# Kernel tuning notes

Hardware: AMD Instinct MI355X
Metric: run time of the kernel (lower is better)

Reference implementation:

```python
import jax, jax.numpy as jnp
import numpy as np

N_HEAD = 16
EPS = 1e-6

def hypersphere_norm(x, g):
    # unit-normalize on hidden dim, rescale to sqrt(d), learnable gain
    d = x.shape[-1]
    n = jnp.linalg.norm(x, axis=-1, keepdims=True)
    return (x / (n + EPS)) * jnp.sqrt(jnp.asarray(d, x.dtype)) * g


def setup_inputs() -> dict:
    key = jax.random.key(0)
    ks = jax.random.split(key, 8)
    B, S, D, F = 2, 2048, 2048, 8192
    s = lambda fan: 1.0 / np.sqrt(fan)
    return {
        "hidden_states": jax.random.normal(ks[0], (B, S, D), jnp.float32),
        "Wq": jax.random.normal(ks[1], (D, D), jnp.float32) * s(D),
        "Wk": jax.random.normal(ks[2], (D, D), jnp.float32) * s(D),
        "Wv": jax.random.normal(ks[3], (D, D), jnp.float32) * s(D),
        "Wo": jax.random.normal(ks[4], (D, D), jnp.float32) * s(D),
        "W_in": jax.random.normal(ks[5], (F, D), jnp.float32) * s(D),
        "W_out": jax.random.normal(ks[6], (D, F), jnp.float32) * s(F),
        "qk_norm_factor": jnp.asarray(1.0 / np.sqrt(D // N_HEAD), jnp.float32),
        "g_attn": jnp.ones((D,), jnp.float32),
        "g_mlp": jnp.ones((D,), jnp.float32),
    }


def reference(hidden_states, Wq, Wk, Wv, Wo, W_in, W_out, qk_norm_factor, g_attn, g_mlp):
    B, S, D = hidden_states.shape
    H = N_HEAD
    hd = D // H

    # ---- pre-attn hypersphere norm ----
    residual = hidden_states
    x = hypersphere_norm(hidden_states, g_attn)

    def shape_heads(t):  # [B,S,D] -> [B,H,S,hd]
        return t.reshape(B, S, H, hd).transpose(0, 2, 1, 3)

    q = shape_heads(x @ Wq.T)
    k = shape_heads(x @ Wk.T)
    v = shape_heads(x @ Wv.T)

    # QK-norm: unit-normalize per head vector
    q = q / (jnp.linalg.norm(q, axis=-1, keepdims=True) + EPS)
    k = k / (jnp.linalg.norm(k, axis=-1, keepdims=True) + EPS)

    scores = jnp.einsum("bhqd,bhkd->bhqk", q, k) * qk_norm_factor
    causal = jnp.tril(jnp.ones((S, S), bool))
    scores = jnp.where(causal[None, None], scores, jnp.asarray(-jnp.inf, scores.dtype))
    probs = jax.nn.softmax(scores, axis=-1)
    attn = jnp.einsum("bhqk,bhkd->bhqd", probs, v)  # [B,H,S,hd]
    attn = attn.transpose(0, 2, 1, 3).reshape(B, S, D)
    attn = attn @ Wo.T  # dropout=0

    h = residual + attn

    # ---- MLP branch ----
    residual = h
    y = hypersphere_norm(h, g_mlp)
    y = jax.nn.gelu(y @ W_in.T, approximate=False)
    y = y @ W_out.T
    return residual + y
```

## Files before the change

### kernel.cpp

```cpp
#include <hip/hip_runtime.h>
#include <math.h>


typedef unsigned short ushort_t;
typedef __attribute__((ext_vector_type(8))) short short8;
typedef __attribute__((ext_vector_type(4))) short short4v;
typedef __attribute__((ext_vector_type(4))) float f32x4;

#define S_LEN 2048
#define D_DIM 2048
#define F_DIM 8192
#define NHEAD 16
#define HDIM 128
#define BATCH 2
#define MROWS (BATCH * S_LEN)

__device__ __forceinline__ float bf2f(ushort_t u) {
  union { unsigned int i; float f; } c; c.i = ((unsigned int)u) << 16; return c.f;
}
__device__ __forceinline__ ushort_t f2bf(float f) {
  union { unsigned int i; float f; } c; c.f = f;
  unsigned int u = c.i;
  unsigned int r = (u + 0x7FFFu + ((u >> 16) & 1u)) >> 16;
  return (ushort_t)r;
}
__device__ __forceinline__ void load_lds16(const ushort_t* g, ushort_t* l) {
  __builtin_amdgcn_global_load_lds((const __attribute__((address_space(1))) void*)g,
                                   (__attribute__((address_space(3))) void*)l,
                                   16, 0, 0);
}
__device__ __forceinline__ f32x4 mf(short8 a, short8 b, f32x4 c) {
  return __builtin_amdgcn_mfma_f32_16x16x32_bf16(a, b, c, 0, 0, 0);
}

__global__ __launch_bounds__(256) void f2b_all_kernel(const float* __restrict__ wq,
                                                      const float* __restrict__ wk,
                                                      const float* __restrict__ wv,
                                                      const float* __restrict__ wo,
                                                      const float* __restrict__ wi,
                                                      const float* __restrict__ wu,
                                                      ushort_t* __restrict__ out) {
  const size_t DD = (size_t)D_DIM * D_DIM;
  const size_t FD = (size_t)F_DIM * D_DIM;
  const size_t e = ((size_t)blockIdx.x * 256 + threadIdx.x) * 4;
  const float* src;
  size_t off;
  if (e < 4 * DD) {
    const int wsel = (int)(e >> 22);
    src = (wsel == 0) ? wq : (wsel == 1) ? wk : (wsel == 2) ? wv : wo;
    off = e & (DD - 1);
  } else if (e < 4 * DD + FD) {
    src = wi; off = e - 4 * DD;
  } else {
    src = wu; off = e - 4 * DD - FD;
  }
  float4 v = *(const float4*)(src + off);
  short4v o;
  o[0] = (short)f2bf(v.x); o[1] = (short)f2bf(v.y);
  o[2] = (short)f2bf(v.z); o[3] = (short)f2bf(v.w);
  *(short4v*)(out + e) = o;
}

__global__ __launch_bounds__(256) void hsnorm_kernel(const float* __restrict__ x,
                                                     const float* __restrict__ g,
                                                     ushort_t* __restrict__ out) {
  const int row = blockIdx.x;
  const int t = threadIdx.x;
  const size_t base = (size_t)row * D_DIM + t * 8;
  float4 x0 = *(const float4*)(x + base);
  float4 x1 = *(const float4*)(x + base + 4);
  float f[8] = {x0.x, x0.y, x0.z, x0.w, x1.x, x1.y, x1.z, x1.w};
  float ss = 0.f;
#pragma unroll
  for (int j = 0; j < 8; ++j) ss += f[j] * f[j];
#pragma unroll
  for (int o = 32; o >= 1; o >>= 1) ss += __shfl_xor(ss, o);
  __shared__ float red[4];
  if ((t & 63) == 0) red[t >> 6] = ss;
  __syncthreads();
  const float tot = red[0] + red[1] + red[2] + red[3];
  const float factor = 45.254833995939045f / (sqrtf(tot) + 1e-6f);
  float4 g0 = *(const float4*)(g + t * 8);
  float4 g1 = *(const float4*)(g + t * 8 + 4);
  float gg[8] = {g0.x, g0.y, g0.z, g0.w, g1.x, g1.y, g1.z, g1.w};
  short8 ov;
#pragma unroll
  for (int j = 0; j < 8; ++j) ov[j] = (short)f2bf(f[j] * factor * gg[j]);
  *(short8*)(out + base) = ov;
}

__global__ __launch_bounds__(256) void qknorm_kernel(ushort_t* __restrict__ buf, float scale) {
  const int wv = threadIdx.x >> 6;
  const int lane = threadIdx.x & 63;
  const size_t vi = (size_t)blockIdx.x * 4 + wv;
  ushort_t* p = buf + vi * 128 + lane * 2;
  const float a = bf2f(p[0]), b = bf2f(p[1]);
  float ss = a * a + b * b;
#pragma unroll
  for (int o = 32; o >= 1; o >>= 1) ss += __shfl_xor(ss, o);
  const float f = scale / (sqrtf(ss) + 1e-6f);
  p[0] = f2bf(a * f);
  p[1] = f2bf(b * f);
}

template <int EPI>
__global__ __launch_bounds__(512, 2) void gemm256(const ushort_t* __restrict__ A,
                                                  const ushort_t* __restrict__ W,
                                                  const float* __restrict__ RES,
                                                  void* __restrict__ Cv,
                                                  int M, int N, int K) {
  extern __shared__ char smem[];
  const int tid = threadIdx.x;
  const int w = tid >> 6;
  const int lane = tid & 63;
  const int quad = lane >> 4;
  const int l15 = lane & 15;
  const int wr = w >> 2, wc = w & 3;

  const int bid = blockIdx.x;
  const int cpx = gridDim.x >> 3;
  const int wg = (bid & 7) * cpx + (bid >> 3);
  const long bm = (long)(wg & 15) * 256;
  const long bn = (long)(wg >> 4) * 256;

  const int rx = (l15 >> 1) & 3;
  const int a_base = ((wr * 128 + l15) << 6) + ((quad ^ rx) << 4);
  const int b_base = ((wc * 64 + l15) << 6) + ((quad ^ rx) << 4);

  const int sp = (((tid & 3) ^ ((tid >> 3) & 3)) << 3);
  const int srow = tid >> 2;
  const ushort_t* gA = A + (size_t)(bm + srow) * K + sp;
  const ushort_t* gB = W + (size_t)(bn + srow) * K + sp;
  const size_t rstep = (size_t)128 * K;
  const int sdst = w * 1024;

#define STAGE(BI, STEP)                                                     \
  {                                                                         \
    char* ab = smem + (BI)*16384;                                           \
    char* bb = smem + 65536 + (BI)*16384;                                   \
    const ushort_t* ga = gA + (size_t)(STEP) * 32;                          \
    const ushort_t* gb = gB + (size_t)(STEP) * 32;                          \
    load_lds16(ga, (ushort_t*)(ab + sdst));                                 \
    load_lds16(ga + rstep, (ushort_t*)(ab + 8192 + sdst));                  \
    load_lds16(gb, (ushort_t*)(bb + sdst));                                 \
    load_lds16(gb + rstep, (ushort_t*)(bb + 8192 + sdst));                  \
  }

  f32x4 acc[8][4] = {};
  short8 af[4], bf[4];
  const int NT = K >> 5;

  STAGE(0, 0);
  STAGE(1, 1);
  STAGE(2, 2);
  asm volatile("s_waitcnt vmcnt(8)" ::: "memory");
  __builtin_amdgcn_s_barrier();

  for (int s = 0; s < NT; ++s) {
    const char* sa = smem + (s & 3) * 16384;
    const char* sb = smem + 65536 + (s & 3) * 16384;
#pragma unroll
    for (int j = 0; j < 4; ++j) bf[j] = *(const short8*)(sb + b_base + j * 1024);
#pragma unroll
    for (int i = 0; i < 4; ++i) af[i] = *(const short8*)(sa + a_base + i * 1024);
    if (s + 3 < NT) STAGE((s + 3) & 3, s + 3);
    __builtin_amdgcn_s_setprio(1);
#pragma unroll
    for (int i = 0; i < 4; ++i)
#pragma unroll
      for (int j = 0; j < 4; ++j) acc[i][j] = mf(af[i], bf[j], acc[i][j]);
    __builtin_amdgcn_s_setprio(0);
#pragma unroll
    for (int i = 0; i < 4; ++i) af[i] = *(const short8*)(sa + a_base + (4 + i) * 1024);
    __builtin_amdgcn_s_setprio(1);
#pragma unroll
    for (int i = 0; i < 4; ++i)
#pragma unroll
      for (int j = 0; j < 4; ++j) acc[4 + i][j] = mf(af[i], bf[j], acc[4 + i][j]);
    __builtin_amdgcn_s_setprio(0);
    if (s < NT - 3) {
      asm volatile("s_waitcnt vmcnt(8)" ::: "memory");
    } else if (s == NT - 3) {
      asm volatile("s_waitcnt vmcnt(4)" ::: "memory");
    } else {
      asm volatile("s_waitcnt vmcnt(0)" ::: "memory");
    }
    __builtin_amdgcn_s_barrier();
  }
#undef STAGE

  const size_t SZq = (size_t)MROWS * D_DIM;
#pragma unroll
  for (int i = 0; i < 8; ++i) {
    const long row0 = bm + wr * 128 + i * 16 + quad * 4;
#pragma unroll
    for (int j = 0; j < 4; ++j) {
      const long col = bn + wc * 64 + j * 16 + l15;
      if (EPI == 4) {
        if (col < 4096) {
          ushort_t* dst = (ushort_t*)Cv + (col < 2048 ? 0 : SZq);
          const long c = col & (D_DIM - 1);
#pragma unroll
          for (int r = 0; r < 4; ++r)
            dst[(size_t)(row0 + r) * D_DIM + c] = f2bf(acc[i][j][r]);
        } else {
          const long b = row0 >> 11;
          const long s0 = row0 & (S_LEN - 1);
          const long h = (col >> 7) & 15;
          const long d = col & (HDIM - 1);
          short4v ov;
#pragma unroll
          for (int r = 0; r < 4; ++r) ov[r] = (short)f2bf(acc[i][j][r]);
          *(short4v*)((ushort_t*)Cv + 2 * SZq + ((b * NHEAD + h) * HDIM + d) * S_LEN + s0) = ov;
        }
      } else {
#pragma unroll
        for (int r = 0; r < 4; ++r) {
          float v = acc[i][j][r];
          const size_t idx = (size_t)(row0 + r) * N + col;
          if (EPI == 1) {
            ((float*)Cv)[idx] = v + RES[idx];
          } else if (EPI == 2) {
            v = 0.5f * v * (1.0f + erff(v * 0.70710678118654752f));
            ((ushort_t*)Cv)[idx] = f2bf(v);
          }
        }
      }
    }
  }
}

__global__ __launch_bounds__(256) void attn_kernel(const ushort_t* __restrict__ q,
                                                   const ushort_t* __restrict__ k,
                                                   const ushort_t* __restrict__ vt,
                                                   ushort_t* __restrict__ out) {
  __shared__ __align__(16) ushort_t K_lds[64 * 128];
  __shared__ __align__(16) ushort_t Vt_lds[128 * 64];
  __shared__ __align__(16) ushort_t P_lds[4 * 16 * 64];
  const int tid = threadIdx.x;
  const int w = tid >> 6;
  const int lane = tid & 63;
  const int quad = lane >> 4;
  const int l15 = lane & 15;

  const int qt = (S_LEN / 64 - 1) - (blockIdx.x & (S_LEN / 64 - 1));
  const int bh = blockIdx.x >> 5;
  const int b = bh >> 4;
  const int h = bh & 15;
  const int q0 = qt * 64;
  const int wrow0 = q0 + w * 16;
  const size_t base = ((size_t)b * S_LEN) * D_DIM + h * HDIM;
  const size_t vtbase = ((size_t)(b * NHEAD + h)) * HDIM * S_LEN;

  short8 qa[4];
#pragma unroll
  for (int st = 0; st < 4; ++st)
    qa[st] = *(const short8*)(q + base + (size_t)(wrow0 + l15) * D_DIM + st * 32 + quad * 8);

  const int kc0 = w * 64 + lane;
  ushort_t* Pw = P_lds + w * 1024;

  f32x4 o[8] = {};
  float m[4], l[4];
#pragma unroll
  for (int r = 0; r < 4; ++r) { m[r] = -__builtin_inff(); l[r] = 0.f; }

  const int ktmax = (q0 + 63) >> 6;
  for (int kt = 0; kt <= ktmax; ++kt) {
#pragma unroll
    for (int r2 = 0; r2 < 4; ++r2) {
      const int c = r2 * 256 + kc0;
      {
        const int db = c >> 8, key = (c >> 2) & 63, dl = (c & 3) * 8;
        load_lds16(k + base + (size_t)(kt * 64 + key) * D_DIM + db * 32 + dl,
                   K_lds + (size_t)(r2 * 4 + w) * 512);
      }
      {
        const int kc = c >> 9, d = (c >> 2) & 127, kl = (c & 3) * 8;
        load_lds16(vt + vtbase + (size_t)d * S_LEN + kt * 64 + kc * 32 + kl,
                   Vt_lds + (size_t)(r2 * 4 + w) * 512);
      }
    }
    __syncthreads();

    if (kt * 64 <= wrow0 + 15) {
      f32x4 s[4];
#pragma unroll
      for (int h2 = 0; h2 < 4; ++h2) {
        f32x4 sa = {};
#pragma unroll
        for (int st = 0; st < 4; ++st) {
          short8 kb = *(const short8*)&K_lds[st * 2048 + (h2 * 16 + l15) * 32 + quad * 8];
          sa = __builtin_amdgcn_mfma_f32_16x16x32_bf16(qa[st], kb, sa, 0, 0, 0);
        }
        s[h2] = sa;
      }

      const int kbase = kt * 64 + l15;
      float alpha[4];
#pragma unroll
      for (int r = 0; r < 4; ++r) {
        const int qrow = wrow0 + quad * 4 + r;
        float sv[4];
#pragma unroll
        for (int h2 = 0; h2 < 4; ++h2)
          sv[h2] = (kbase + h2 * 16 <= qrow) ? s[h2][r] : -__builtin_inff();
        float tmax = fmaxf(fmaxf(sv[0], sv[1]), fmaxf(sv[2], sv[3]));
#pragma unroll
        for (int off = 8; off >= 1; off >>= 1) tmax = fmaxf(tmax, __shfl_xor(tmax, off));
        const float mn = fmaxf(m[r], tmax);
        const float al = __expf(m[r] - mn);
        float p[4], ps = 0.f;
#pragma unroll
        for (int h2 = 0; h2 < 4; ++h2) { p[h2] = __expf(sv[h2] - mn); ps += p[h2]; }
#pragma unroll
        for (int off = 8; off >= 1; off >>= 1) ps += __shfl_xor(ps, off);
        l[r] = l[r] * al + ps;
        m[r] = mn;
        alpha[r] = al;
#pragma unroll
        for (int h2 = 0; h2 < 4; ++h2)
          Pw[(h2 >> 1) * 512 + (quad * 4 + r) * 32 + (h2 & 1) * 16 + l15] = f2bf(p[h2]);
      }

#pragma unroll
      for (int c = 0; c < 8; ++c)
#pragma unroll
        for (int r = 0; r < 4; ++r) o[c][r] *= alpha[r];

      short8 af0 = *(const short8*)&Pw[l15 * 32 + quad * 8];
      short8 af1 = *(const short8*)&Pw[512 + l15 * 32 + quad * 8];
#pragma unroll
      for (int c = 0; c < 8; ++c) {
        short8 vb0 = *(const short8*)&Vt_lds[(c * 16 + l15) * 32 + quad * 8];
        o[c] = __builtin_amdgcn_mfma_f32_16x16x32_bf16(af0, vb0, o[c], 0, 0, 0);
        short8 vb1 = *(const short8*)&Vt_lds[4096 + (c * 16 + l15) * 32 + quad * 8];
        o[c] = __builtin_amdgcn_mfma_f32_16x16x32_bf16(af1, vb1, o[c], 0, 0, 0);
      }
    }
    __syncthreads();
  }

#pragma unroll
  for (int c = 0; c < 8; ++c)
#pragma unroll
    for (int r = 0; r < 4; ++r) {
      const float val = o[c][r] / l[r];
      out[base + (size_t)(wrow0 + quad * 4 + r) * D_DIM + c * 16 + l15] = f2bf(val);
    }
}

extern "C" void kernel_launch(void* const* d_in, const int* in_sizes, int n_in,
                              void* d_out, int out_size, void* d_ws, size_t ws_size,
                              hipStream_t stream) {
  const float* hid  = (const float*)d_in[0];
  const float* Wq   = (const float*)d_in[1];
  const float* Wk   = (const float*)d_in[2];
  const float* Wv   = (const float*)d_in[3];
  const float* Wo   = (const float*)d_in[4];
  const float* Win  = (const float*)d_in[5];
  const float* Wout = (const float*)d_in[6];
  const float* ga   = (const float*)d_in[8];
  const float* gm   = (const float*)d_in[9];
  float* out = (float*)d_out;

  const size_t DD = (size_t)D_DIM * D_DIM;
  const size_t FD = (size_t)F_DIM * D_DIM;
  const size_t SZ = (size_t)MROWS * D_DIM;

  ushort_t* wqb  = (ushort_t*)d_ws;
  ushort_t* wob  = wqb + 3 * DD;
  ushort_t* winb = wob + DD;
  ushort_t* woutb= winb + FD;
  float*    hb   = (float*)(woutb + FD);
  ushort_t* qb   = (ushort_t*)(hb + SZ);
  ushort_t* kb   = qb + SZ;
  ushort_t* vtb  = kb + SZ;
  ushort_t* xb   = vtb + SZ;
  ushort_t* mid  = kb;

  static int attr_set = 0;
  if (!attr_set) {
    hipFuncSetAttribute((const void*)&gemm256<1>,
                        hipFuncAttributeMaxDynamicSharedMemorySize, 131072);
    hipFuncSetAttribute((const void*)&gemm256<2>,
                        hipFuncAttributeMaxDynamicSharedMemorySize, 131072);
    hipFuncSetAttribute((const void*)&gemm256<4>,
                        hipFuncAttributeMaxDynamicSharedMemorySize, 131072);
    attr_set = 1;
  }

  f2b_all_kernel<<<(unsigned)((4 * DD + 2 * FD) / 1024), 256, 0, stream>>>(
      Wq, Wk, Wv, Wo, Win, Wout, wqb);

  hsnorm_kernel<<<MROWS, 256, 0, stream>>>(hid, ga, xb);
  gemm256<4><<<(MROWS / 256) * (6144 / 256), 512, 131072, stream>>>(
      xb, wqb, nullptr, qb, MROWS, 6144, D_DIM);
  qknorm_kernel<<<(MROWS * NHEAD) / 4, 256, 0, stream>>>(qb, 0.08838834764831845f);
  qknorm_kernel<<<(MROWS * NHEAD) / 4, 256, 0, stream>>>(kb, 1.0f);
  attn_kernel<<<BATCH * NHEAD * (S_LEN / 64), 256, 0, stream>>>(qb, kb, vtb, xb);
  gemm256<1><<<(MROWS / 256) * (D_DIM / 256), 512, 131072, stream>>>(
      xb, wob, hid, hb, MROWS, D_DIM, D_DIM);
  hsnorm_kernel<<<MROWS, 256, 0, stream>>>(hb, gm, qb);
  gemm256<2><<<(MROWS / 256) * (F_DIM / 256), 512, 131072, stream>>>(
      qb, winb, nullptr, mid, MROWS, F_DIM, D_DIM);
  gemm256<1><<<(MROWS / 256) * (D_DIM / 256), 512, 131072, stream>>>(
      mid, woutb, hb, out, MROWS, D_DIM, F_DIM);
}
```

Before: 1.011 ms.

## Interleave global-to-LDS loads with MFMA pairs and drop XCD block remapping

The GEMM main loop now issues its four global-to-LDS prefetch loads one at a time between groups of two MFMA rows. Before, all four went out in a burst before the compute. The A fragments are loaded two at a time, which lowers register pressure. The XCD-aware swizzle of the 1D block index is replaced by a plain 2D grid with blockIdx.x for M and blockIdx.y for N. That may change how L2 is shared across chiplets, so reuse could get better or worse.

```diff
diff --git a/kernel.cpp b/kernel.cpp
--- a/kernel.cpp
+++ b/kernel.cpp
@@ -116,12 +116,8 @@
   const int quad = lane >> 4;
   const int l15 = lane & 15;
   const int wr = w >> 2, wc = w & 3;
-
-  const int bid = blockIdx.x;
-  const int cpx = gridDim.x >> 3;
-  const int wg = (bid & 7) * cpx + (bid >> 3);
-  const long bm = (long)(wg & 15) * 256;
-  const long bn = (long)(wg >> 4) * 256;
+  const long bm = (long)blockIdx.x * 256;
+  const long bn = (long)blockIdx.y * 256;
 
   const int rx = (l15 >> 1) & 3;
   const int a_base = ((wr * 128 + l15) << 6) + ((quad ^ rx) << 4);
@@ -134,7 +130,10 @@
   const size_t rstep = (size_t)128 * K;
   const int sdst = w * 1024;
 
-#define STAGE(BI, STEP)                                                     \
+  f32x4 acc[8][4] = {};
+  const int NT = K >> 5;
+
+#define STAGE4(BI, STEP)                                                    \
   {                                                                         \
     char* ab = smem + (BI)*16384;                                           \
     char* bb = smem + 65536 + (BI)*16384;                                   \
@@ -146,38 +145,57 @@
     load_lds16(gb + rstep, (ushort_t*)(bb + 8192 + sdst));                  \
   }
 
-  f32x4 acc[8][4] = {};
-  short8 af[4], bf[4];
-  const int NT = K >> 5;
-
-  STAGE(0, 0);
-  STAGE(1, 1);
-  STAGE(2, 2);
+  STAGE4(0, 0);
+  STAGE4(1, 1);
+  STAGE4(2, 2);
   asm volatile("s_waitcnt vmcnt(8)" ::: "memory");
   __builtin_amdgcn_s_barrier();
+
+#define MROW2(R0, R1)                                                       \
+  {                                                                         \
+    __builtin_amdgcn_s_setprio(1);                                          \
+    acc[R0][0] = mf(a0, b0, acc[R0][0]);                                    \
+    acc[R0][1] = mf(a0, b1, acc[R0][1]);                                    \
+    acc[R0][2] = mf(a0, b2, acc[R0][2]);                                    \
+    acc[R0][3] = mf(a0, b3, acc[R0][3]);                                    \
+    acc[R1][0] = mf(a1, b0, acc[R1][0]);                                    \
+    acc[R1][1] = mf(a1, b1, acc[R1][1]);                                    \
+    acc[R1][2] = mf(a1, b2, acc[R1][2]);                                    \
+    acc[R1][3] = mf(a1, b3, acc[R1][3]);                                    \
+    __builtin_amdgcn_s_setprio(0);                                          \
+  }
 
   for (int s = 0; s < NT; ++s) {
     const char* sa = smem + (s & 3) * 16384;
     const char* sb = smem + 65536 + (s & 3) * 16384;
-#pragma unroll
-    for (int j = 0; j < 4; ++j) bf[j] = *(const short8*)(sb + b_base + j * 1024);
-#pragma unroll
-    for (int i = 0; i < 4; ++i) af[i] = *(const short8*)(sa + a_base + i * 1024);
-    if (s + 3 < NT) STAGE((s + 3) & 3, s + 3);
-    __builtin_amdgcn_s_setprio(1);
-#pragma unroll
-    for (int i = 0; i < 4; ++i)
-#pragma unroll
-      for (int j = 0; j < 4; ++j) acc[i][j] = mf(af[i], bf[j], acc[i][j]);
-    __builtin_amdgcn_s_setprio(0);
-#pragma unroll
-    for (int i = 0; i < 4; ++i) af[i] = *(const short8*)(sa + a_base + (4 + i) * 1024);
-    __builtin_amdgcn_s_setprio(1);
-#pragma unroll
-    for (int i = 0; i < 4; ++i)
-#pragma unroll
-      for (int j = 0; j < 4; ++j) acc[4 + i][j] = mf(af[i], bf[j], acc[4 + i][j]);
-    __builtin_amdgcn_s_setprio(0);
+    const bool more = (s + 3 < NT);
+    const int bi = (s + 3) & 3;
+    char* ab = smem + bi * 16384;
+    char* bb = smem + 65536 + bi * 16384;
+    const ushort_t* ga = gA + (size_t)(s + 3) * 32;
+    const ushort_t* gb = gB + (size_t)(s + 3) * 32;
+
+    short8 b0 = *(const short8*)(sb + b_base);
+    short8 b1 = *(const short8*)(sb + b_base + 1024);
+    short8 b2 = *(const short8*)(sb + b_base + 2048);
+    short8 b3 = *(const short8*)(sb + b_base + 3072);
+    short8 a0 = *(const short8*)(sa + a_base);
+    short8 a1 = *(const short8*)(sa + a_base + 1024);
+    if (more) load_lds16(ga, (ushort_t*)(ab + sdst));
+    MROW2(0, 1);
+    a0 = *(const short8*)(sa + a_base + 2048);
+    a1 = *(const short8*)(sa + a_base + 3072);
+    if (more) load_lds16(ga + rstep, (ushort_t*)(ab + 8192 + sdst));
+    MROW2(2, 3);
+    a0 = *(const short8*)(sa + a_base + 4096);
+    a1 = *(const short8*)(sa + a_base + 5120);
+    if (more) load_lds16(gb, (ushort_t*)(bb + sdst));
+    MROW2(4, 5);
+    a0 = *(const short8*)(sa + a_base + 6144);
+    a1 = *(const short8*)(sa + a_base + 7168);
+    if (more) load_lds16(gb + rstep, (ushort_t*)(bb + 8192 + sdst));
+    MROW2(6, 7);
+
     if (s < NT - 3) {
       asm volatile("s_waitcnt vmcnt(8)" ::: "memory");
     } else if (s == NT - 3) {
@@ -187,7 +205,8 @@
     }
     __builtin_amdgcn_s_barrier();
   }
-#undef STAGE
+#undef MROW2
+#undef STAGE4
 
   const size_t SZq = (size_t)MROWS * D_DIM;
 #pragma unroll
@@ -394,16 +413,16 @@
       Wq, Wk, Wv, Wo, Win, Wout, wqb);
 
   hsnorm_kernel<<<MROWS, 256, 0, stream>>>(hid, ga, xb);
-  gemm256<4><<<(MROWS / 256) * (6144 / 256), 512, 131072, stream>>>(
+  gemm256<4><<<dim3(MROWS / 256, 6144 / 256), 512, 131072, stream>>>(
       xb, wqb, nullptr, qb, MROWS, 6144, D_DIM);
   qknorm_kernel<<<(MROWS * NHEAD) / 4, 256, 0, stream>>>(qb, 0.08838834764831845f);
   qknorm_kernel<<<(MROWS * NHEAD) / 4, 256, 0, stream>>>(kb, 1.0f);
   attn_kernel<<<BATCH * NHEAD * (S_LEN / 64), 256, 0, stream>>>(qb, kb, vtb, xb);
-  gemm256<1><<<(MROWS / 256) * (D_DIM / 256), 512, 131072, stream>>>(
+  gemm256<1><<<dim3(MROWS / 256, D_DIM / 256), 512, 131072, stream>>>(
       xb, wob, hid, hb, MROWS, D_DIM, D_DIM);
   hsnorm_kernel<<<MROWS, 256, 0, stream>>>(hb, gm, qb);
-  gemm256<2><<<(MROWS / 256) * (F_DIM / 256), 512, 131072, stream>>>(
+  gemm256<2><<<dim3(MROWS / 256, F_DIM / 256), 512, 131072, stream>>>(
       qb, winb, nullptr, mid, MROWS, F_DIM, D_DIM);
-  gemm256<1><<<(MROWS / 256) * (D_DIM / 256), 512, 131072, stream>>>(
+  gemm256<1><<<dim3(MROWS / 256, D_DIM / 256), 512, 131072, stream>>>(
       mid, woutb, hb, out, MROWS, D_DIM, F_DIM);
 }
```

New measurement: 976.0 us. 1.04x faster.
